# Optimization experiments

Measured on AMD Instinct MI355X. Metric: run time of the kernel, lower is better.

Reference implementation:

```python
import jax, jax.numpy as jnp
import numpy as np


def setup_inputs() -> dict:
    key = jax.random.key(0)
    k1, k2 = jax.random.split(key)
    # x: [B, emb_dim, H, W] encoder features; embed: [emb_dim, dict_size] codebook
    x = jax.random.normal(k1, (32, 256, 32, 32), dtype=jnp.float32)
    embed = jax.random.normal(k2, (256, 8192), dtype=jnp.float32)
    return {"x": x, "embed": embed}


def reference(x, embed):
    B, C, H, W = x.shape  # C == emb_dim
    # torch transpose(1, -1) swaps dims 1 and 3 -> [B, W, H, C]
    flatten = jnp.transpose(x, (0, 3, 2, 1)).reshape(-1, C)  # [N, C], N = B*W*H
    # L2 distance via expansion: ||e||^2 + ||z||^2 - 2 z e  -> [N, dict_size]
    dist = (jnp.sum(embed * embed, axis=0)[None, :]
            + jnp.sum(flatten * flatten, axis=1, keepdims=True)
            - 2.0 * flatten @ embed)
    # nearest codebook id per vector; original views ids back as input shape minus dim 1
    ids = jnp.argmin(dist, axis=1).reshape(B, H, W)  # int ids, [B, H, W]
    # embedding lookup from embed.T ([dict_size, C]) -> [B, H, W, C]
    vqs = embed.T[ids]
    # torch transpose(1, -1) on 4D -> [B, C, W, H] (matches x since H == W)
    vqs = jnp.transpose(vqs, (0, 3, 2, 1))
    # straight-through estimator: forward value = vqs, grad w.r.t. x = identity
    out = vqs + x - jax.lax.stop_gradient(x)
    return out, ids
```

## Files before the change

### kernel.cpp

```cpp
#include <hip/hip_runtime.h>
#include <math.h>

typedef float f32x4 __attribute__((ext_vector_type(4)));
typedef __attribute__((ext_vector_type(8))) short short8;

#define C_DIM  256
#define K_DIM  8192
#define HW     1024
#define N_ROWS 32768
#define N_OUT  8388608
#define TAU    0.75f

__device__ __forceinline__ unsigned short f2bf(float v) {
    union { float f; unsigned u; } a; a.f = v;
    unsigned r = a.u + 0x7fffu + ((a.u >> 16) & 1u);
    return (unsigned short)(r >> 16);
}
__device__ __forceinline__ float bf2f(unsigned short b) {
    union { float f; unsigned u; } a; a.u = ((unsigned)b) << 16; return a.f;
}

__global__ void enorm_kernel(const float* __restrict__ embed, float* __restrict__ e_norm) {
    int k = blockIdx.x * 256 + threadIdx.x;
    float s = 0.f;
    #pragma unroll 8
    for (int c = 0; c < C_DIM; ++c) { float v = embed[c * K_DIM + k]; s = __builtin_fmaf(v, v, s); }
    e_norm[k] = s;
}

__global__ void z2_kernel(const float* __restrict__ x, float* __restrict__ z2) {
    int r = blockIdx.x * 256 + threadIdx.x;
    int b = r >> 10, t = r & 1023;
    const float* xb = x + b * (C_DIM * HW) + t;
    float s = 0.f;
    #pragma unroll 8
    for (int c = 0; c < C_DIM; ++c) { float v = xb[c << 10]; s = __builtin_fmaf(v, v, s); }
    z2[r] = s;
}

__global__ void prepA_kernel(const float* __restrict__ x, unsigned short* __restrict__ abuf) {
    int u = blockIdx.x * 256 + threadIdx.x;
    int l = u & 63;
    int f = (u >> 6) & 15;
    int ck = (u >> 10) & 7;
    int blk = u >> 13;
    int row = (blk << 8) + (f << 4) + (l & 15);
    int ch0 = (ck << 5) + ((l >> 4) << 3);
    int b = row >> 10, t = row & 1023;
    const float* xp = x + ((size_t)((b << 8) + ch0) << 10) + t;
    short8 hi;
    #pragma unroll
    for (int j = 0; j < 8; ++j) hi[j] = (short)f2bf(xp[(size_t)j << 10]);
    *(short8*)(abuf + (size_t)u * 8) = hi;
}

__global__ void prepE_kernel(const float* __restrict__ embed, unsigned short* __restrict__ ebuf) {
    int u = blockIdx.x * 256 + threadIdx.x;
    int l = u & 63;
    int f = (u >> 6) & 3;
    int s = (u >> 8) & 1;
    int ck = (u >> 9) & 7;
    int nt = u >> 12;
    int col = (nt << 6) + (f << 4) + (l & 15);
    int ch0 = (ck << 5) + ((l >> 4) << 3);
    short8 w;
    #pragma unroll
    for (int j = 0; j < 8; ++j) {
        float v = embed[(size_t)(ch0 + j) * K_DIM + col];
        unsigned short h = f2bf(v);
        w[j] = (short)(s ? f2bf(v - bf2f(h)) : h);
    }
    *(short8*)(ebuf + (size_t)u * 8) = w;
}

#define GLDS(S, D) __builtin_amdgcn_global_load_lds(                              \
        (const __attribute__((address_space(1))) void*)(S),                       \
        (__attribute__((address_space(3))) void*)(D), 16, 0, 0)

__launch_bounds__(512, 2)
__global__ void vq_main(const unsigned short* __restrict__ abuf,
                        const unsigned short* __restrict__ ebuf,
                        const float* __restrict__ e_norm,
                        float4* __restrict__ res) {
    __shared__ unsigned short ldsA[57344];
    __shared__ unsigned short ldsE[2][8192];
    const int tid  = threadIdx.x;
    const int lane = tid & 63;
    const int wid  = tid >> 6;
    const int wm   = wid >> 1, wn = wid & 1;
    const int mtB  = blockIdx.x >> 1, nh = blockIdx.x & 1;
    const unsigned short* aSlab = abuf + (size_t)mtB * 65536u;

    #pragma unroll
    for (int i = 0; i < 14; ++i)
        GLDS(aSlab + i * 4096 + tid * 8, ldsA + i * 4096 + tid * 8);

    #define STAGE_E(NTL, KK, BUF) do {                                                        \
        GLDS(ebuf + ((size_t)(nh * 64 + (NTL)) * 32768u) + (KK) * 4096 + tid * 8,             \
             &ldsE[BUF][tid * 8]);                                                            \
        GLDS(ebuf + ((size_t)(nh * 64 + 32 + (NTL)) * 32768u) + (KK) * 4096 + tid * 8,        \
             &ldsE[BUF][4096 + tid * 8]);                                                     \
    } while (0)

    STAGE_E(0, 0, 0);

    short8 a7[4];
    #pragma unroll
    for (int mi = 0; mi < 4; ++mi)
        a7[mi] = *(const short8*)(aSlab + 57344 + (wm * 4 + mi) * 512 + lane * 8);

    float d1[16], d2[16]; int i1[16], i2[16];
    #pragma unroll
    for (int s = 0; s < 16; ++s) { d1[s] = INFINITY; d2[s] = INFINITY; i1[s] = 0; i2[s] = 0; }

    asm volatile("s_waitcnt vmcnt(0)" ::: "memory");
    __syncthreads();

    int cur = 0;
    #pragma unroll 1
    for (int ntl = 0; ntl < 32; ++ntl) {
        const int colb = nh * 4096 + wn * 2048 + ntl * 64 + (lane & 15);
        float e2v[4];
        #pragma unroll
        for (int cf = 0; cf < 4; ++cf) e2v[cf] = e_norm[colb + cf * 16];

        f32x4 acc[4][4];
        #pragma unroll
        for (int mi = 0; mi < 4; ++mi)
            #pragma unroll
            for (int cf = 0; cf < 4; ++cf) acc[mi][cf] = (f32x4){0.f, 0.f, 0.f, 0.f};

        #pragma unroll
        for (int kk = 0; kk < 8; ++kk) {
            const int np = ntl * 8 + kk + 1;
            if (np < 256) STAGE_E(np >> 3, np & 7, cur ^ 1);

            short8 ah[4];
            if (kk < 7) {
                #pragma unroll
                for (int mi = 0; mi < 4; ++mi)
                    ah[mi] = *(const short8*)(ldsA + kk * 8192 + (wm * 4 + mi) * 512 + lane * 8);
            } else {
                #pragma unroll
                for (int mi = 0; mi < 4; ++mi) ah[mi] = a7[mi];
            }
            short8 eh[4], el[4];
            #pragma unroll
            for (int cf = 0; cf < 4; ++cf) {
                eh[cf] = *(const short8*)(&ldsE[cur][wn * 4096 + cf * 512 + lane * 8]);
                el[cf] = *(const short8*)(&ldsE[cur][wn * 4096 + 2048 + cf * 512 + lane * 8]);
            }
            #pragma unroll
            for (int cf = 0; cf < 4; ++cf)
                #pragma unroll
                for (int mi = 0; mi < 4; ++mi) {
                    acc[mi][cf] = __builtin_amdgcn_mfma_f32_16x16x32_bf16(ah[mi], eh[cf], acc[mi][cf], 0, 0, 0);
                    acc[mi][cf] = __builtin_amdgcn_mfma_f32_16x16x32_bf16(ah[mi], el[cf], acc[mi][cf], 0, 0, 0);
                }
            asm volatile("s_waitcnt vmcnt(0)" ::: "memory");
            __syncthreads();
            cur ^= 1;
        }

        #pragma unroll
        for (int cf = 0; cf < 4; ++cf) {
            const int idx = colb + cf * 16;
            #pragma unroll
            for (int mi = 0; mi < 4; ++mi)
                #pragma unroll
                for (int r = 0; r < 4; ++r) {
                    const int s = mi * 4 + r;
                    float d = __builtin_fmaf(-2.f, acc[mi][cf][r], e2v[cf]);
                    bool b1 = d < d1[s];
                    bool b2 = d < d2[s];
                    d2[s] = b1 ? d1[s] : (b2 ? d : d2[s]);
                    i2[s] = b1 ? i1[s] : (b2 ? idx : i2[s]);
                    d1[s] = b1 ? d : d1[s];
                    i1[s] = b1 ? idx : i1[s];
                }
        }
    }

    #pragma unroll
    for (int s = 0; s < 16; ++s) {
        float a1 = d1[s], a2 = d2[s]; int x1 = i1[s], x2 = i2[s];
        #pragma unroll
        for (int m = 1; m < 8; m <<= 1) {
            float o1 = __shfl_xor(a1, m, 64), o2 = __shfl_xor(a2, m, 64);
            int  oi1 = __shfl_xor(x1, m, 64), oi2 = __shfl_xor(x2, m, 64);
            bool ow = (o1 < a1) || (o1 == a1 && oi1 < x1);
            float w1v = ow ? o1 : a1; int w1i = ow ? oi1 : x1;
            float l1  = ow ? a1 : o1; int l1i = ow ? x1 : oi1;
            float c2  = ow ? o2 : a2; int c2i = ow ? oi2 : x2;
            bool sw = (c2 < l1) || (c2 == l1 && c2i < l1i);
            a1 = w1v; x1 = w1i;
            a2 = sw ? c2 : l1; x2 = sw ? c2i : l1i;
        }
        d1[s] = a1; d2[s] = a2; i1[s] = x1; i2[s] = x2;
    }
    if ((lane & 7) == 0) {
        const int lst = (lane >> 3) & 1;
        const int h = lane >> 4;
        const int slot = nh * 4 + wn * 2 + lst;
        #pragma unroll
        for (int mi = 0; mi < 4; ++mi)
            #pragma unroll
            for (int r = 0; r < 4; ++r) {
                const int s = mi * 4 + r;
                int row = mtB * 256 + wm * 64 + mi * 16 + h * 4 + r;
                float4 v; v.x = d1[s]; v.y = d2[s];
                v.z = __int_as_float(i1[s]); v.w = __int_as_float(i2[s]);
                res[row * 8 + slot] = v;
            }
    }
    #undef STAGE_E
}

__global__ void merge_kernel(const float* __restrict__ x, const float* __restrict__ embed,
                             const float* __restrict__ e_norm, const float* __restrict__ z2,
                             const float4* __restrict__ res, int* __restrict__ ids_final) {
    int row = blockIdx.x * 256 + threadIdx.x;
    float4 v[8];
    #pragma unroll
    for (int j = 0; j < 8; ++j) v[j] = res[row * 8 + j];
    float w1 = INFINITY; int wi = 0x7fffffff;
    #pragma unroll
    for (int j = 0; j < 8; ++j) {
        float d = v[j].x; int i = __float_as_int(v[j].z);
        if (d < w1 || (d == w1 && i < wi)) { w1 = d; wi = i; }
    }
    float w2 = INFINITY;
    #pragma unroll
    for (int j = 0; j < 8; ++j) {
        if (__float_as_int(v[j].z) != wi && v[j].x < w2) w2 = v[j].x;
        if (__float_as_int(v[j].w) != wi && v[j].y < w2) w2 = v[j].y;
    }
    int id = wi;
    if (w2 - w1 <= TAU) {
        float zz = z2[row];
        int b = row >> 10, t = row & 1023;
        const float* xb = x + ((size_t)b << 18) + t;
        float bd = INFINITY; int bi = 0x7fffffff;
        float thr = w1 + TAU;
        #pragma unroll
        for (int j = 0; j < 8; ++j)
            #pragma unroll
            for (int sl = 0; sl < 2; ++sl) {
                float dap = sl ? v[j].y : v[j].x;
                int k = __float_as_int(sl ? v[j].w : v[j].z);
                if (dap <= thr) {
                    float dot = 0.f;
                    for (int c = 0; c < C_DIM; ++c)
                        dot = __builtin_fmaf(xb[(size_t)c << 10], embed[((size_t)c << 13) + k], dot);
                    float dd = __fadd_rn(__fadd_rn(e_norm[k], zz), -__fmul_rn(2.0f, dot));
                    if (dd < bd || (dd == bd && k < bi)) { bd = dd; bi = k; }
                }
            }
        id = bi;
    }
    ids_final[row] = id;
}

__global__ void out_kernel(const float* __restrict__ embed, const int* __restrict__ ids_final,
                           float* __restrict__ out, float* __restrict__ ids_out) {
    const int blk = blockIdx.x;
    const int b = blk >> 4, t0 = (blk & 15) << 6;
    const int tid = threadIdx.x;
    const int t_off = tid & 63, w4 = tid >> 6;

    if (tid < 64) {
        int t = t0 + tid;
        int id = ids_final[(b << 10) + t];
        int n = (b << 10) + ((t & 31) << 5) + (t >> 5);
        ids_out[n] = (float)id;
    }
    const int myid = ids_final[(b << 10) + t0 + t_off];
    const float* ecol = embed + myid;
    float* ob = out + b * (C_DIM * HW) + t0 + t_off;
    #pragma unroll 4
    for (int c = w4; c < C_DIM; c += 4)
        ob[c * HW] = ecol[c * K_DIM];
}

extern "C" void kernel_launch(void* const* d_in, const int* in_sizes, int n_in,
                              void* d_out, int out_size, void* d_ws, size_t ws_size,
                              hipStream_t stream) {
    const float* x     = (const float*)d_in[0];
    const float* embed = (const float*)d_in[1];
    float* out = (float*)d_out;
    float* ids_out = out + N_OUT;

    unsigned short* abuf = (unsigned short*)d_out;
    float4* res = (float4*)((char*)d_out + (16u << 20));

    unsigned short* ebuf = (unsigned short*)d_ws;
    float* e_norm   = (float*)((char*)d_ws + (8u << 20));
    float* z2       = e_norm + K_DIM;
    int*   ids_final = (int*)(z2 + N_ROWS);

    enorm_kernel<<<K_DIM / 256, 256, 0, stream>>>(embed, e_norm);
    z2_kernel<<<N_ROWS / 256, 256, 0, stream>>>(x, z2);
    prepA_kernel<<<4096, 256, 0, stream>>>(x, abuf);
    prepE_kernel<<<2048, 256, 0, stream>>>(embed, ebuf);
    vq_main<<<256, 512, 0, stream>>>(abuf, ebuf, e_norm, res);
    merge_kernel<<<N_ROWS / 256, 256, 0, stream>>>(x, embed, e_norm, z2, res, ids_final);
    out_kernel<<<512, 256, 0, stream>>>(embed, ids_final, out, ids_out);
}
```

Before: 560.4 us.

## Triple-buffer codebook staging, LDS-transpose prep kernels, drop z2, gather via transposed embed

Main GEMM moves from a double to a triple E buffer, staging two steps ahead with a partial vmcnt wait and a raw barrier. It also raises MFMA priority and moves the e_norm load inside the kk loop. The prep kernels now transpose through LDS for coalesced reads, and the e_norm computation is folded into prepE. The z2 kernel is removed, since ||z||^2 is constant per row and does not affect the argmin. When workspace allows, a transposed embed copy is written so the output gather reads contiguous rows and writes through an LDS transpose. These changes cut launches and uncoalesced traffic, at the cost of more LDS and an extra 8MB write.

```diff
diff --git a/kernel.cpp b/kernel.cpp
--- a/kernel.cpp
+++ b/kernel.cpp
@@ -20,57 +20,83 @@
     union { float f; unsigned u; } a; a.u = ((unsigned)b) << 16; return a.f;
 }
 
-__global__ void enorm_kernel(const float* __restrict__ embed, float* __restrict__ e_norm) {
-    int k = blockIdx.x * 256 + threadIdx.x;
-    float s = 0.f;
+
+__global__ void prepA_kernel(const float* __restrict__ x, unsigned short* __restrict__ abuf) {
+    __shared__ float ldsT[256 * 65];
+    const int tid = threadIdx.x;
+    const int b = blockIdx.x >> 4, tq = blockIdx.x & 15;
+    const int t0 = tq << 6;
+    const int l = tid & 63, q = tid >> 6;
+    const float* xb = x + ((size_t)b << 18) + t0;
     #pragma unroll 8
-    for (int c = 0; c < C_DIM; ++c) { float v = embed[c * K_DIM + k]; s = __builtin_fmaf(v, v, s); }
-    e_norm[k] = s;
-}
-
-__global__ void z2_kernel(const float* __restrict__ x, float* __restrict__ z2) {
-    int r = blockIdx.x * 256 + threadIdx.x;
-    int b = r >> 10, t = r & 1023;
-    const float* xb = x + b * (C_DIM * HW) + t;
-    float s = 0.f;
+    for (int cg = 0; cg < 64; ++cg) {
+        int c = (cg << 2) + q;
+        ldsT[c * 65 + l] = xb[((size_t)c << 10) + l];
+    }
+    __syncthreads();
+    const int slabblk = (b << 2) + (tq >> 2);
+    const int fbase = (tq & 3) << 2;
+    #pragma unroll
+    for (int i = 0; i < 8; ++i) {
+        int unit = (i << 2) + q;
+        int ck = unit >> 2, fsub = unit & 3;
+        int toff = (fsub << 4) + (l & 15);
+        int ch0 = (ck << 5) + ((l >> 4) << 3);
+        short8 hi;
+        #pragma unroll
+        for (int j = 0; j < 8; ++j) hi[j] = (short)f2bf(ldsT[(ch0 + j) * 65 + toff]);
+        size_t base = (((size_t)slabblk * 8 + ck) * 16 + fbase + fsub) * 512 + l * 8;
+        *(short8*)(abuf + base) = hi;
+    }
+}
+
+__global__ void prepE_kernel(const float* __restrict__ embed, unsigned short* __restrict__ ebuf,
+                             float* __restrict__ e_norm, float* __restrict__ embedT) {
+    __shared__ float ldsT[256 * 65];
+    __shared__ float pnorm[256];
+    const int tid = threadIdx.x;
+    const int kq = blockIdx.x;
+    const int col0 = kq << 6;
+    const int l = tid & 63, q = tid >> 6;
     #pragma unroll 8
-    for (int c = 0; c < C_DIM; ++c) { float v = xb[c << 10]; s = __builtin_fmaf(v, v, s); }
-    z2[r] = s;
-}
-
-__global__ void prepA_kernel(const float* __restrict__ x, unsigned short* __restrict__ abuf) {
-    int u = blockIdx.x * 256 + threadIdx.x;
-    int l = u & 63;
-    int f = (u >> 6) & 15;
-    int ck = (u >> 10) & 7;
-    int blk = u >> 13;
-    int row = (blk << 8) + (f << 4) + (l & 15);
-    int ch0 = (ck << 5) + ((l >> 4) << 3);
-    int b = row >> 10, t = row & 1023;
-    const float* xp = x + ((size_t)((b << 8) + ch0) << 10) + t;
-    short8 hi;
-    #pragma unroll
-    for (int j = 0; j < 8; ++j) hi[j] = (short)f2bf(xp[(size_t)j << 10]);
-    *(short8*)(abuf + (size_t)u * 8) = hi;
-}
-
-__global__ void prepE_kernel(const float* __restrict__ embed, unsigned short* __restrict__ ebuf) {
-    int u = blockIdx.x * 256 + threadIdx.x;
-    int l = u & 63;
-    int f = (u >> 6) & 3;
-    int s = (u >> 8) & 1;
-    int ck = (u >> 9) & 7;
-    int nt = u >> 12;
-    int col = (nt << 6) + (f << 4) + (l & 15);
-    int ch0 = (ck << 5) + ((l >> 4) << 3);
-    short8 w;
-    #pragma unroll
-    for (int j = 0; j < 8; ++j) {
-        float v = embed[(size_t)(ch0 + j) * K_DIM + col];
-        unsigned short h = f2bf(v);
-        w[j] = (short)(s ? f2bf(v - bf2f(h)) : h);
-    }
-    *(short8*)(ebuf + (size_t)u * 8) = w;
+    for (int cg = 0; cg < 64; ++cg) {
+        int c = (cg << 2) + q;
+        ldsT[c * 65 + l] = embed[((size_t)c << 13) + col0 + l];
+    }
+    __syncthreads();
+    {
+        float s = 0.f;
+        #pragma unroll 8
+        for (int cc = 0; cc < 64; ++cc) {
+            float v = ldsT[(q * 64 + cc) * 65 + l];
+            s = __builtin_fmaf(v, v, s);
+        }
+        pnorm[q * 64 + l] = s;
+    }
+    __syncthreads();
+    if (tid < 64)
+        e_norm[col0 + tid] = (pnorm[tid] + pnorm[64 + tid]) + (pnorm[128 + tid] + pnorm[192 + tid]);
+    #pragma unroll
+    for (int i = 0; i < 16; ++i) {
+        int unit = (i << 2) + q;
+        int f = unit & 3, s = (unit >> 2) & 1, ck = unit >> 3;
+        int coff = (f << 4) + (l & 15);
+        int ch0 = (ck << 5) + ((l >> 4) << 3);
+        short8 w;
+        #pragma unroll
+        for (int j = 0; j < 8; ++j) {
+            float v = ldsT[(ch0 + j) * 65 + coff];
+            unsigned short h = f2bf(v);
+            w[j] = (short)(s ? f2bf(v - bf2f(h)) : h);
+        }
+        size_t base = ((((size_t)kq * 8 + ck) * 2 + s) * 4 + f) * 512 + l * 8;
+        *(short8*)(ebuf + base) = w;
+    }
+    if (embedT) {
+        #pragma unroll 8
+        for (int i = 0; i < 64; ++i)
+            embedT[(size_t)(col0 + i) * 256 + tid] = ldsT[tid * 65 + i];
+    }
 }
 
 #define GLDS(S, D) __builtin_amdgcn_global_load_lds(                              \
@@ -82,8 +108,8 @@
                         const unsigned short* __restrict__ ebuf,
                         const float* __restrict__ e_norm,
                         float4* __restrict__ res) {
-    __shared__ unsigned short ldsA[57344];
-    __shared__ unsigned short ldsE[2][8192];
+    __shared__ unsigned short ldsA[49152];
+    __shared__ unsigned short ldsE[3][8192];
     const int tid  = threadIdx.x;
     const int lane = tid & 63;
     const int wid  = tid >> 6;
@@ -91,10 +117,6 @@
     const int mtB  = blockIdx.x >> 1, nh = blockIdx.x & 1;
     const unsigned short* aSlab = abuf + (size_t)mtB * 65536u;
 
-    #pragma unroll
-    for (int i = 0; i < 14; ++i)
-        GLDS(aSlab + i * 4096 + tid * 8, ldsA + i * 4096 + tid * 8);
-
     #define STAGE_E(NTL, KK, BUF) do {                                                        \
         GLDS(ebuf + ((size_t)(nh * 64 + (NTL)) * 32768u) + (KK) * 4096 + tid * 8,             \
              &ldsE[BUF][tid * 8]);                                                            \
@@ -102,12 +124,17 @@
              &ldsE[BUF][4096 + tid * 8]);                                                     \
     } while (0)
 
+    #pragma unroll
+    for (int i = 0; i < 12; ++i)
+        GLDS(aSlab + i * 4096 + tid * 8, ldsA + i * 4096 + tid * 8);
     STAGE_E(0, 0, 0);
 
-    short8 a7[4];
-    #pragma unroll
-    for (int mi = 0; mi < 4; ++mi)
-        a7[mi] = *(const short8*)(aSlab + 57344 + (wm * 4 + mi) * 512 + lane * 8);
+    short8 a6[4], a7[4];
+    #pragma unroll
+    for (int mi = 0; mi < 4; ++mi) {
+        a6[mi] = *(const short8*)(aSlab + 6 * 8192 + (wm * 4 + mi) * 512 + lane * 8);
+        a7[mi] = *(const short8*)(aSlab + 7 * 8192 + (wm * 4 + mi) * 512 + lane * 8);
+    }
 
     float d1[16], d2[16]; int i1[16], i2[16];
     #pragma unroll
@@ -115,15 +142,13 @@
 
     asm volatile("s_waitcnt vmcnt(0)" ::: "memory");
     __syncthreads();
+    STAGE_E(0, 1, 1);
 
     int cur = 0;
     #pragma unroll 1
     for (int ntl = 0; ntl < 32; ++ntl) {
         const int colb = nh * 4096 + wn * 2048 + ntl * 64 + (lane & 15);
         float e2v[4];
-        #pragma unroll
-        for (int cf = 0; cf < 4; ++cf) e2v[cf] = e_norm[colb + cf * 16];
-
         f32x4 acc[4][4];
         #pragma unroll
         for (int mi = 0; mi < 4; ++mi)
@@ -132,24 +157,41 @@
 
         #pragma unroll
         for (int kk = 0; kk < 8; ++kk) {
-            const int np = ntl * 8 + kk + 1;
-            if (np < 256) STAGE_E(np >> 3, np & 7, cur ^ 1);
+            if (kk == 7 && ntl == 31) { asm volatile("s_waitcnt vmcnt(0)" ::: "memory"); }
+            else                      { asm volatile("s_waitcnt vmcnt(2)" ::: "memory"); }
+            __builtin_amdgcn_s_barrier();
+            asm volatile("" ::: "memory");
+
+            if (kk == 0) {
+                #pragma unroll
+                for (int cf = 0; cf < 4; ++cf) e2v[cf] = e_norm[colb + cf * 16];
+            }
+            const int np = ntl * 8 + kk + 2;
+            if (np < 256) {
+                int nb = cur + 2; if (nb >= 3) nb -= 3;
+                STAGE_E(np >> 3, np & 7, nb);
+            }
 
             short8 ah[4];
-            if (kk < 7) {
+            if (kk < 6) {
                 #pragma unroll
                 for (int mi = 0; mi < 4; ++mi)
                     ah[mi] = *(const short8*)(ldsA + kk * 8192 + (wm * 4 + mi) * 512 + lane * 8);
+            } else if (kk == 6) {
+                #pragma unroll
+                for (int mi = 0; mi < 4; ++mi) ah[mi] = a6[mi];
             } else {
                 #pragma unroll
                 for (int mi = 0; mi < 4; ++mi) ah[mi] = a7[mi];
             }
+            const unsigned short* le = ldsE[cur];
             short8 eh[4], el[4];
             #pragma unroll
             for (int cf = 0; cf < 4; ++cf) {
-                eh[cf] = *(const short8*)(&ldsE[cur][wn * 4096 + cf * 512 + lane * 8]);
-                el[cf] = *(const short8*)(&ldsE[cur][wn * 4096 + 2048 + cf * 512 + lane * 8]);
-            }
+                eh[cf] = *(const short8*)(le + wn * 4096 + cf * 512 + lane * 8);
+                el[cf] = *(const short8*)(le + wn * 4096 + 2048 + cf * 512 + lane * 8);
+            }
+            __builtin_amdgcn_s_setprio(1);
             #pragma unroll
             for (int cf = 0; cf < 4; ++cf)
                 #pragma unroll
@@ -157,9 +199,8 @@
                     acc[mi][cf] = __builtin_amdgcn_mfma_f32_16x16x32_bf16(ah[mi], eh[cf], acc[mi][cf], 0, 0, 0);
                     acc[mi][cf] = __builtin_amdgcn_mfma_f32_16x16x32_bf16(ah[mi], el[cf], acc[mi][cf], 0, 0, 0);
                 }
-            asm volatile("s_waitcnt vmcnt(0)" ::: "memory");
-            __syncthreads();
-            cur ^= 1;
+            __builtin_amdgcn_s_setprio(0);
+            cur = (cur == 2) ? 0 : cur + 1;
         }
 
         #pragma unroll
@@ -202,12 +243,13 @@
         const int lst = (lane >> 3) & 1;
         const int h = lane >> 4;
         const int slot = nh * 4 + wn * 2 + lst;
+        const int rowbase = (mtB << 8) + wm * 64 + (h << 2);
         #pragma unroll
         for (int mi = 0; mi < 4; ++mi)
             #pragma unroll
             for (int r = 0; r < 4; ++r) {
                 const int s = mi * 4 + r;
-                int row = mtB * 256 + wm * 64 + mi * 16 + h * 4 + r;
+                int row = rowbase + mi * 16 + r;
                 float4 v; v.x = d1[s]; v.y = d2[s];
                 v.z = __int_as_float(i1[s]); v.w = __int_as_float(i2[s]);
                 res[row * 8 + slot] = v;
@@ -217,7 +259,7 @@
 }
 
 __global__ void merge_kernel(const float* __restrict__ x, const float* __restrict__ embed,
-                             const float* __restrict__ e_norm, const float* __restrict__ z2,
+                             const float* __restrict__ e_norm,
                              const float4* __restrict__ res, int* __restrict__ ids_final) {
     int row = blockIdx.x * 256 + threadIdx.x;
     float4 v[8];
@@ -237,7 +279,6 @@
     }
     int id = wi;
     if (w2 - w1 <= TAU) {
-        float zz = z2[row];
         int b = row >> 10, t = row & 1023;
         const float* xb = x + ((size_t)b << 18) + t;
         float bd = INFINITY; int bi = 0x7fffffff;
@@ -252,13 +293,46 @@
                     float dot = 0.f;
                     for (int c = 0; c < C_DIM; ++c)
                         dot = __builtin_fmaf(xb[(size_t)c << 10], embed[((size_t)c << 13) + k], dot);
-                    float dd = __fadd_rn(__fadd_rn(e_norm[k], zz), -__fmul_rn(2.0f, dot));
+                    float dd = __fadd_rn(e_norm[k], -__fmul_rn(2.0f, dot));
                     if (dd < bd || (dd == bd && k < bi)) { bd = dd; bi = k; }
                 }
             }
         id = bi;
     }
     ids_final[row] = id;
+}
+
+__global__ void outT_kernel(const float* __restrict__ embedT, const int* __restrict__ ids_final,
+                            float* __restrict__ out, float* __restrict__ ids_out) {
+    __shared__ float fo[64 * 257];
+    __shared__ int idsl[64];
+    const int blk = blockIdx.x;
+    const int b = blk >> 4, t0 = (blk & 15) << 6;
+    const int tid = threadIdx.x;
+    const int l = tid & 63, q = tid >> 6;
+    if (tid < 64) {
+        int t = t0 + tid;
+        int id = ids_final[(b << 10) + t];
+        idsl[tid] = id;
+        int n = (b << 10) + ((t & 31) << 5) + (t >> 5);
+        ids_out[n] = (float)id;
+    }
+    __syncthreads();
+    #pragma unroll
+    for (int i = 0; i < 16; ++i) {
+        int slot = (i << 2) + q;
+        const float* src = embedT + (size_t)idsl[slot] * 256;
+        #pragma unroll
+        for (int seg = 0; seg < 4; ++seg)
+            fo[slot * 257 + (seg << 6) + l] = src[(seg << 6) + l];
+    }
+    __syncthreads();
+    float* ob = out + ((size_t)b << 18) + t0;
+    #pragma unroll 8
+    for (int ci = 0; ci < 64; ++ci) {
+        int c = (ci << 2) + q;
+        ob[((size_t)c << 10) + l] = fo[l * 257 + c];
+    }
 }
 
 __global__ void out_kernel(const float* __restrict__ embed, const int* __restrict__ ids_final,
@@ -267,7 +341,6 @@
     const int b = blk >> 4, t0 = (blk & 15) << 6;
     const int tid = threadIdx.x;
     const int t_off = tid & 63, w4 = tid >> 6;
-
     if (tid < 64) {
         int t = t0 + tid;
         int id = ids_final[(b << 10) + t];
@@ -294,15 +367,16 @@
     float4* res = (float4*)((char*)d_out + (16u << 20));
 
     unsigned short* ebuf = (unsigned short*)d_ws;
-    float* e_norm   = (float*)((char*)d_ws + (8u << 20));
-    float* z2       = e_norm + K_DIM;
-    int*   ids_final = (int*)(z2 + N_ROWS);
-
-    enorm_kernel<<<K_DIM / 256, 256, 0, stream>>>(embed, e_norm);
-    z2_kernel<<<N_ROWS / 256, 256, 0, stream>>>(x, z2);
-    prepA_kernel<<<4096, 256, 0, stream>>>(x, abuf);
-    prepE_kernel<<<2048, 256, 0, stream>>>(embed, ebuf);
+    float* e_norm    = (float*)((char*)d_ws + 8388608u);
+    int*   ids_final = (int*)((char*)d_ws + 8388608u + 32768u);
+    size_t embT_off  = 8388608u + 32768u + 131072u;
+    bool useT = (ws_size >= embT_off + 8388608u);
+    float* embedT = useT ? (float*)((char*)d_ws + embT_off) : nullptr;
+
+    prepA_kernel<<<512, 256, 0, stream>>>(x, abuf);
+    prepE_kernel<<<128, 256, 0, stream>>>(embed, ebuf, e_norm, embedT);
     vq_main<<<256, 512, 0, stream>>>(abuf, ebuf, e_norm, res);
-    merge_kernel<<<N_ROWS / 256, 256, 0, stream>>>(x, embed, e_norm, z2, res, ids_final);
-    out_kernel<<<512, 256, 0, stream>>>(embed, ids_final, out, ids_out);
-}
+    merge_kernel<<<N_ROWS / 256, 256, 0, stream>>>(x, embed, e_norm, res, ids_final);
+    if (useT) outT_kernel<<<512, 256, 0, stream>>>(embedT, ids_final, out, ids_out);
+    else      out_kernel<<<512, 256, 0, stream>>>(embed, ids_final, out, ids_out);
+}
```

New measurement: 533.1 us. -4.9%, faster.
